# Kernel tuning notes

Measured on AMD Instinct MI355X. Metric: run time of the kernel, lower is better.

## Reference

```python
import jax, jax.numpy as jnp
import numpy as np
import math

# init config (matches init_kwargs); sigma/alpha are squared in __init__
SIGMA2 = 8.0 ** 2
ALPHA2 = 8.0 ** 2
C_SIZE = 512
STRIDE = 8
MINX = 1e-06
M = 100                      # ratio=100 > 1 -> M = int(ratio), capped at 100
K = C_SIZE // STRIDE         # 64 grid cells per axis
G = K * K                    # 4096 density-field cells
B, N = 8, 512                # images, annotated points per image
TWO_PI = 2.0 * math.pi


def setup_inputs():
    key = jax.random.key(0)
    k1, _ = jax.random.split(key)
    points = jax.random.uniform(k1, (B, N, 2), dtype=jnp.float32) * C_SIZE
    st_sizes = jnp.full((B,), float(C_SIZE), dtype=jnp.float32)
    return {"points": points, "st_sizes": st_sizes}


def _per_image(pts, cood):
    # pts: [N,2]; cood: [K]
    x = pts[:, 0]
    y = pts[:, 1]
    dx = x[:, None] - cood[None, :]                 # [N,K]
    dy = y[:, None] - cood[None, :]                 # [N,K]
    # dis_all = y_dis[:, :, None] + x_dis[:, None, :] flattened: g = iy*K + ix
    dis = (dy[:, :, None] ** 2 + dx[:, None, :] ** 2).reshape(pts.shape[0], G)  # [N,G]
    s1 = ALPHA2 + SIGMA2
    s2 = ALPHA2 + SIGMA2 / 2.0
    m = jnp.exp(-0.5 / s1 * dis) / (TWO_PI * s1)    # [N,G]
    tv = jnp.exp(-0.5 / s2 * dis) / (TWO_PI * s2)
    v = (tv / (TWO_PI * 2.0 * SIGMA2)).sum(0) - (m ** 2).sum(0)   # [G] (sel_v == v, no bg)
    # top-M cells by sel_v, then sort indices ascending (ratio>1 branch -> static M)
    inds = jnp.argsort(-v)
    Minds = jnp.sort(inds[:M])                      # [M]
    v = jnp.maximum(v, MINX)                        # add=False -> clamp
    # xf[n, iy*K+ix] = x_n - cood[ix]; yf[n, iy*K+ix] = y_n - cood[iy]
    iy = Minds // K
    ix = Minds % K
    xfM = dx[:, ix]                                 # [N,M]
    yfM = dy[:, iy]                                 # [N,M]
    df = (xfM[:, None, :] - xfM[:, :, None]) ** 2 + (yfM[:, None, :] - yfM[:, :, None]) ** 2
    af = (0.5 * (xfM[:, None, :] + xfM[:, :, None])) ** 2 + (0.5 * (yfM[:, None, :] + yfM[:, :, None])) ** 2
    g1 = jnp.exp(-0.5 / (2.0 * SIGMA2) * df) / (TWO_PI * 2.0 * SIGMA2)          # [N,M,M]
    tmpv2 = (g1 * (jnp.exp(-0.5 / s2 * af) / (TWO_PI * s2))).sum(0) + g1.sum(0)  # [M,M]
    disM = dis[:, Minds]                            # [N,M]
    tmpm2 = jnp.exp(-0.5 / s1 * disM) / (TWO_PI * s1)
    A = tmpv2 - tmpm2.T @ tmpm2                     # [M,M]
    eye = jnp.eye(M, dtype=bool)
    A = jnp.where(eye, 1e-10, A)                    # diag overwritten to 1e-10
    vM = v[Minds] + 1e-10
    tmpA = vM[:, None] * jnp.linalg.inv(A) * vM[None, :] + jnp.diag(vM)
    Bm = jnp.linalg.inv(tmpA)
    return m, v, A, Bm, Minds


def reference(points, st_sizes):
    # st_sizes only matters for use_background=True; kept for signature fidelity
    cood = jnp.arange(0, C_SIZE, STRIDE, dtype=jnp.float32) + STRIDE / 2.0
    m, v, A, Bm, Minds = jax.vmap(lambda p: _per_image(p, cood))(points)
    return m, v, A, Bm, Minds
```

## Files before the change

### kernel.cpp

```cpp
#include <hip/hip_runtime.h>
#include <math.h>

#ifndef M_PI
#define M_PI 3.14159265358979323846
#endif

#define BB 8
#define NN 512
#define KK 64
#define GG 4096
#define MM 100

#define SZ_VD    (BB*GG*8u*4u)
#define OFF_VD   0u
#define SZ_VM    (BB*MM*4u)
#define OFF_VM   (OFF_VD + SZ_VD)
#define SZ_AD    (BB*MM*MM*4u)
#define OFF_AD   (OFF_VM + SZ_VM)

#define OUT_M  0
#define OUT_V  (BB*NN*GG)
#define OUT_A  (OUT_V + BB*GG)
#define OUT_B  (OUT_A + BB*MM*MM)
#define OUT_MI (OUT_B + BB*MM*MM)

#define MU_PER 8
#define MU_VP 4096
#define MU_AS 2048
#define MU_IV 10240

__device__ __forceinline__ void m_units(const float* __restrict__ pts,
                                        float* __restrict__ out, int u0, int cnt) {
  const float CM = (float)(1.0/(2.0*M_PI*128.0));
  for (int k = 0; k < cnt; ++k) {
    int u = u0 + k;
    int t = u*256 + (int)threadIdx.x;
    int e = t << 2;
    int img = e >> 21;
    int rem = e & ((1 << 21) - 1);
    int n = rem >> 12;
    int g = rem & 4095;
    int iy = g >> 6, ix = g & 63;
    float x = pts[(img*NN + n)*2 + 0];
    float y = pts[(img*NN + n)*2 + 1];
    float dy = y - (8.0f*iy + 4.0f);
    float ey = __expf(dy*dy*(-0.5f/128.0f));
    float4 r;
    float dx0 = x - (8.0f*ix + 4.0f);
    float dx1 = x - (8.0f*(ix+1) + 4.0f);
    float dx2 = x - (8.0f*(ix+2) + 4.0f);
    float dx3 = x - (8.0f*(ix+3) + 4.0f);
    r.x = ey*__expf(dx0*dx0*(-0.5f/128.0f))*CM;
    r.y = ey*__expf(dx1*dx1*(-0.5f/128.0f))*CM;
    r.z = ey*__expf(dx2*dx2*(-0.5f/128.0f))*CM;
    r.w = ey*__expf(dx3*dx3*(-0.5f/128.0f))*CM;
    *reinterpret_cast<float4*>(&out[OUT_M + e]) = r;
  }
}

__device__ __forceinline__ void m_units512(const float* __restrict__ pts,
                                           float* __restrict__ out, int u0, int cnt) {
  const float CM = (float)(1.0/(2.0*M_PI*128.0));
  for (int k = 0; k < cnt/2; ++k) {
    int t = u0*256 + k*512 + (int)threadIdx.x;
    int e = t << 2;
    int img = e >> 21;
    int rem = e & ((1 << 21) - 1);
    int n = rem >> 12;
    int g = rem & 4095;
    int iy = g >> 6, ix = g & 63;
    float x = pts[(img*NN + n)*2 + 0];
    float y = pts[(img*NN + n)*2 + 1];
    float dy = y - (8.0f*iy + 4.0f);
    float ey = __expf(dy*dy*(-0.5f/128.0f));
    float4 r;
    float dx0 = x - (8.0f*ix + 4.0f);
    float dx1 = x - (8.0f*(ix+1) + 4.0f);
    float dx2 = x - (8.0f*(ix+2) + 4.0f);
    float dx3 = x - (8.0f*(ix+3) + 4.0f);
    r.x = ey*__expf(dx0*dx0*(-0.5f/128.0f))*CM;
    r.y = ey*__expf(dx1*dx1*(-0.5f/128.0f))*CM;
    r.z = ey*__expf(dx2*dx2*(-0.5f/128.0f))*CM;
    r.w = ey*__expf(dx3*dx3*(-0.5f/128.0f))*CM;
    *reinterpret_cast<float4*>(&out[OUT_M + e]) = r;
  }
}

__device__ __forceinline__ float flt_readlane(float v, int l) {
  return __int_as_float(__builtin_amdgcn_readlane(__float_as_int(v), l));
}

__global__ __launch_bounds__(256) void k_vpart(const float* __restrict__ pts,
                                               double* __restrict__ vd,
                                               float* __restrict__ out) {
  __shared__ double sEy2[16][66], sEy3[16][66], sEx2[16][66], sEx3[16][66];
  __shared__ float px[128], py[128];
  int bid = blockIdx.x;
  if (bid >= BB*64) { m_units(pts, out, (bid - BB*64)*MU_PER, MU_PER); return; }
  int quarter = bid & 3;
  int rem = bid >> 2;
  int tile = rem & 15;
  int img = rem >> 4;
  int iy0 = (tile >> 2) << 4;
  int ix0 = (tile & 3) << 4;
  int tx = threadIdx.x & 15, ty = threadIdx.x >> 4;
  int n = threadIdx.x & 63;
  int tbl = threadIdx.x >> 6;
  if (threadIdx.x < 128) {
    px[threadIdx.x] = pts[(img*NN + quarter*128 + threadIdx.x)*2 + 0];
    py[threadIdx.x] = pts[(img*NN + quarter*128 + threadIdx.x)*2 + 1];
  }
  const double alpha = (tbl & 1) ? (1.0/128.0) : (0.5/96.0);
  const double Q = exp(-128.0*alpha);
  const int base = (tbl >= 2) ? ix0 : iy0;
  double* dst = (tbl == 0) ? &sEy2[0][0] : (tbl == 1) ? &sEy3[0][0]
              : (tbl == 2) ? &sEx2[0][0] : &sEx3[0][0];
  double aV = 0.0, aM = 0.0;
  for (int kc = 0; kc < 2; ++kc) {
    int nbl = kc << 6;
    __syncthreads();
    {
      int nn = nbl + n;
      double coord = (tbl >= 2) ? (double)px[nn] : (double)py[nn];
      double d0 = coord - (8.0*base + 4.0);
      double E = exp(-alpha*d0*d0);
      double R = exp(alpha*(16.0*d0 - 64.0));
      #pragma unroll
      for (int row = 0; row < 16; ++row) {
        dst[row*66 + n] = E;
        E *= R; R *= Q;
      }
    }
    __syncthreads();
    #pragma unroll 8
    for (int n2 = 0; n2 < 64; n2 += 2) {
      double2 y2 = *reinterpret_cast<const double2*>(&sEy2[ty][n2]);
      double2 x2 = *reinterpret_cast<const double2*>(&sEx2[tx][n2]);
      double2 y3 = *reinterpret_cast<const double2*>(&sEy3[ty][n2]);
      double2 x3 = *reinterpret_cast<const double2*>(&sEx3[tx][n2]);
      aV += y2.x*x2.x; aV += y2.y*x2.y;
      aM += y3.x*x3.x; aM += y3.y*x3.y;
    }
  }
  const double CTV = 1.0/((2.0*M_PI*96.0)*(2.0*M_PI*128.0));
  const double CM2 = 1.0/((2.0*M_PI*128.0)*(2.0*M_PI*128.0));
  vd[quarter*(BB*GG) + img*GG + (iy0 + ty)*KK + ix0 + tx] = CTV*aV - CM2*aM;
}

union AselU {
  struct {
    unsigned int ku[GG];
    unsigned int hist[32][257];
    unsigned int wq[4];
    unsigned int sPref, sMask;
    unsigned int sRem, sPickB, sPickRem, sCGt, sCEq;
    int tie[128];
  } se;
  struct {
    float sxi[16][130], syi[16][130], sti[16][130];
    float sxj[16][130], syj[16][130], stj[16][130];
    float px[NN], py[NN];
    float cxi[16], cyi[16], cxj[16], cyj[16];
  } ka;
};

__device__ __forceinline__ void wave_sort128(int* a) {
  int L = (int)(threadIdx.x & 63);
  int e0 = a[2*L], e1 = a[2*L + 1];
  for (int kk = 2; kk <= 128; kk <<= 1) {
    for (int jj = kk >> 1; jj >= 2; jj >>= 1) {
      int pl = jj >> 1;
      int o0 = __shfl_xor(e0, pl);
      int o1 = __shfl_xor(e1, pl);
      bool upper = (L & pl) != 0;
      bool up = ((2*L) & kk) == 0;
      if (up != upper) { e0 = min(e0, o0); e1 = min(e1, o1); }
      else             { e0 = max(e0, o0); e1 = max(e1, o1); }
    }
    bool up = ((2*L) & kk) == 0;
    int lo = min(e0, e1), hi = max(e0, e1);
    e0 = up ? lo : hi; e1 = up ? hi : lo;
  }
  a[2*L] = e0; a[2*L + 1] = e1;
}

__global__ __launch_bounds__(256) void k_Asel(const float* __restrict__ pts,
                                              const double* __restrict__ vd,
                                              float* __restrict__ out,
                                              float* __restrict__ ad,
                                              float* __restrict__ vm) {
  __shared__ AselU u;
  __shared__ int selFinal[128];
  int bid = blockIdx.x;
  if (bid >= BB*28) { m_units(pts, out, MU_VP + (bid - BB*28)*MU_PER, MU_PER); return; }
  int img = bid / 28;
  int tile = bid - img*28;
  bool tile0 = (tile == 0);
  int tid = threadIdx.x;
  int wv = tid >> 6;
  int lane = tid & 63;
  int hc = tid >> 3;

  for (int t = 0; t < 16; ++t) {
    int g = t*256 + tid;
    float v = (float)(((vd[img*GG + g] + vd[BB*GG + img*GG + g])
                     + vd[2*BB*GG + img*GG + g]) + vd[3*BB*GG + img*GG + g]);
    if (tile0) out[OUT_V + img*GG + g] = fmaxf(v, 1e-6f);
    int w = __float_as_int(v);
    u.se.ku[g] = (w < 0) ? ~(unsigned)w : ((unsigned)w | 0x80000000u);
  }
  if (tid == 0) {
    u.se.sRem = 100; u.se.sPref = 0u; u.se.sMask = 0u;
    u.se.sCGt = 0; u.se.sCEq = 0;
  }
  for (int shift = 24; shift >= 0; shift -= 8) {
    for (int s = tid; s < 32*257; s += 256) (&u.se.hist[0][0])[s] = 0;
    __syncthreads();
    unsigned mask = u.se.sMask, pref = u.se.sPref;
    for (int t = 0; t < 16; ++t) {
      unsigned k = u.se.ku[t*256 + tid];
      if ((k & mask) == pref)
        atomicAdd(&u.se.hist[hc][(k >> shift) & 255u], 1u);
    }
    __syncthreads();
    unsigned tot = 0;
    #pragma unroll
    for (int c = 0; c < 32; ++c) tot += u.se.hist[c][tid];
    unsigned val = tot;
    #pragma unroll
    for (int off = 1; off < 64; off <<= 1) {
      unsigned o = (unsigned)__shfl_down((int)val, off);
      if (lane + off < 64) val += o;
    }
    if (lane == 0) u.se.wq[wv] = val;
    __syncthreads();
    unsigned suf = val;
    for (int w2 = wv + 1; w2 < 4; ++w2) suf += u.se.wq[w2];
    unsigned rem = u.se.sRem;
    unsigned sgt = suf - tot;
    if (suf >= rem && sgt < rem) { u.se.sPickB = (unsigned)tid; u.se.sPickRem = rem - sgt; }
    __syncthreads();
    if (tid == 0) {
      u.se.sPref |= u.se.sPickB << shift;
      u.se.sMask |= 255u << shift;
      u.se.sRem   = u.se.sPickRem;
    }
    __syncthreads();
  }
  unsigned T = u.se.sPref;
  for (int t = 0; t < 16; ++t) {
    int g = t*256 + tid;
    unsigned k = u.se.ku[g];
    if (k > T) {
      unsigned p = atomicAdd(&u.se.sCGt, 1u);
      selFinal[p] = g;
    } else if (k == T) {
      unsigned p = atomicAdd(&u.se.sCEq, 1u);
      if (p < 128) u.se.tie[p] = g;
    }
  }
  __syncthreads();
  unsigned cgt = u.se.sCGt, ceq = u.se.sCEq, r = u.se.sRem;
  if (tid < 128 && tid >= (int)((ceq < 128u) ? ceq : 128u)) u.se.tie[tid] = 0x7fffffff;
  __syncthreads();
  if (tid < 64) wave_sort128(u.se.tie);
  __syncthreads();
  if (tid < (int)r) selFinal[cgt + tid] = u.se.tie[tid];
  if (tid >= MM && tid < 128) selFinal[tid] = 0x7fffffff;
  __syncthreads();
  if (tid < 64) wave_sort128(selFinal);
  __syncthreads();
  if (tile0 && tid < MM) {
    int mi = selFinal[tid];
    out[OUT_MI + img*MM + tid] = (float)mi;
    float vsel = (float)(((vd[img*GG + mi] + vd[BB*GG + img*GG + mi])
                        + vd[2*BB*GG + img*GG + mi]) + vd[3*BB*GG + img*GG + mi]);
    vm[img*MM + tid] = fmaxf(vsel, 1e-6f) + 1e-10f;
  }
  __syncthreads();

  int it = 0, trem = tile;
  while (trem >= 7 - it) { trem -= 7 - it; ++it; }
  int jt = it + trem;
  int i0 = it*16, j0 = jt*16;
  int tj = tid & 15, ti = tid >> 4;
  int i = i0 + ti, j = j0 + tj;
  const float CM = (float)(1.0/(2.0*M_PI*128.0));
  const float C1 = (float)(1.0/(2.0*M_PI*128.0));
  const float C2 = (float)(1.0/(2.0*M_PI*96.0));
  for (int s = tid; s < NN; s += 256) {
    u.ka.px[s] = pts[(img*NN + s)*2 + 0];
    u.ka.py[s] = pts[(img*NN + s)*2 + 1];
  }
  if (tid < 16) {
    int gi = i0 + tid; if (gi > 99) gi = 99;
    int mi = selFinal[gi];
    u.ka.cxi[tid] = 8.0f*(mi & 63) + 4.0f;
    u.ka.cyi[tid] = 8.0f*(mi >> 6) + 4.0f;
  } else if (tid < 32) {
    int rr = tid - 16;
    int gj = j0 + rr; if (gj > 99) gj = 99;
    int mj = selFinal[gj];
    u.ka.cxj[rr] = 8.0f*(mj & 63) + 4.0f;
    u.ka.cyj[rr] = 8.0f*(mj >> 6) + 4.0f;
  }
  float aV = 0.0f, aM = 0.0f;
  for (int nc = 0; nc < NN; nc += 128) {
    __syncthreads();
    for (int s = tid; s < 16*128; s += 256) {
      int row = s >> 7, n = s & 127;
      float x = u.ka.px[nc + n], y = u.ka.py[nc + n];
      float fxi = x - u.ka.cxi[row], fyi = y - u.ka.cyi[row];
      u.ka.sxi[row][n] = fxi; u.ka.syi[row][n] = fyi;
      u.ka.sti[row][n] = __expf((fxi*fxi + fyi*fyi)*(-0.5f/128.0f))*CM;
      float fxj = x - u.ka.cxj[row], fyj = y - u.ka.cyj[row];
      u.ka.sxj[row][n] = fxj; u.ka.syj[row][n] = fyj;
      u.ka.stj[row][n] = __expf((fxj*fxj + fyj*fyj)*(-0.5f/128.0f))*CM;
    }
    __syncthreads();
    #pragma unroll 4
    for (int n = 0; n < 128; ++n) {
      float xi = u.ka.sxi[ti][n], yi = u.ka.syi[ti][n], tii = u.ka.sti[ti][n];
      float xj = u.ka.sxj[tj][n], yj = u.ka.syj[tj][n], tjj = u.ka.stj[tj][n];
      float ddx = xj - xi, ddy = yj - yi;
      float df = ddx*ddx + ddy*ddy;
      float sx = 0.5f*(xi + xj), sy = 0.5f*(yi + yj);
      float af = sx*sx + sy*sy;
      float g1 = __expf(df*(-0.5f/128.0f))*C1;
      float h  = __expf(af*(-0.5f/96.0f))*C2;
      aV += g1 + g1*h;
      aM += tii*tjj;
    }
  }
  if (i < 100 && j < 100) {
    float val = (i == j) ? 1e-10f : (float)((double)aV - (double)aM);
    out[OUT_A + (img*MM + i)*MM + j] = val;
    ad[(img*MM + i)*MM + j] = val;
    if (it != jt) {
      out[OUT_A + (img*MM + j)*MM + i] = val;
      ad[(img*MM + j)*MM + i] = val;
    }
  }
}

#define PRS 130
__global__ __launch_bounds__(512)
void k_inv_m(const float* __restrict__ ad,
             const float* __restrict__ vm,
             const float* __restrict__ pts,
             float* __restrict__ out) {
  __shared__ float S[128*17];
  __shared__ float Pr[16*PRS];
  __shared__ float svm[112];
  if (blockIdx.x >= BB) {
    m_units512(pts, out, MU_VP + MU_AS + ((int)blockIdx.x - BB)*MU_PER, MU_PER);
    return;
  }
  int img = blockIdx.x;
  int tx = threadIdx.x & 31, ty = threadIdx.x >> 5;
  float C[7][4];
  if (threadIdx.x < 100) svm[threadIdx.x] = vm[img*MM + threadIdx.x];
  #pragma unroll
  for (int a = 0; a < 7; ++a) {
    int r = ty + 16*a;
    #pragma unroll
    for (int b = 0; b < 4; ++b) {
      int col = tx + 32*b;
      float v2 = (r < 100 && col < 100) ? ad[(img*MM + r)*MM + col] : 0.0f;
      if (r == col && r < 100) v2 += vm[img*MM + r];
      C[a][b] = v2;
    }
  }
  for (int p = 0; p < 7; ++p) {
    int k0 = p*16;
    int nbp = (p == 6) ? 4 : 16;
    {
      int bp = p >> 1;
      bool mine = ((tx >> 4) == (p & 1));
      int cq = tx & 15;
      #pragma unroll
      for (int a = 0; a < 7; ++a) {
        int r = ty + 16*a;
        if (mine) {
          float val = 0.0f;
          #pragma unroll
          for (int b = 0; b < 4; ++b) if (b == bp) val = C[a][b];
          S[r*17 + cq] = (r < 100 && cq < nbp) ? val : 0.0f;
        }
      }
    }
    {
      float pv[4];
      #pragma unroll
      for (int b = 0; b < 4; ++b) pv[b] = 0.0f;
      #pragma unroll
      for (int a = 0; a < 7; ++a) {
        #pragma unroll
        for (int b = 0; b < 4; ++b) if (a == p) pv[b] = C[a][b];
      }
      #pragma unroll
      for (int b = 0; b < 4; ++b) Pr[ty*PRS + tx + 32*b] = pv[b];
    }
    __syncthreads();
    if (threadIdx.x < 64) {
      int lane = threadIdx.x;
      float P0[16], P1[16];
      #pragma unroll
      for (int c = 0; c < 16; ++c) {
        P0[c] = S[lane*17 + c];
        P1[c] = (lane + 64 < 112) ? S[(lane + 64)*17 + c] : 0.0f;
      }
      #pragma unroll
      for (int kk = 0; kk < 16; ++kk) {
        if (kk < nbp) {
          int kg = k0 + kk;
          int r1 = lane + 64;
          bool khigh = kg >= 64; int kl = kg & 63;
          float pivinv = 1.0f / flt_readlane(khigh ? P1[kk] : P0[kk], kl);
          float pr[16];
          #pragma unroll
          for (int c = 0; c < 16; ++c) {
            float pv = flt_readlane(khigh ? P1[c] : P0[c], kl);
            pr[c] = (c == kk) ? pivinv : pv*pivinv;
          }
          {
            float f = P0[kk];
            if (lane == kg) {
              #pragma unroll
              for (int c = 0; c < 16; ++c) P0[c] = pr[c];
            } else {
              #pragma unroll
              for (int c = 0; c < 16; ++c) P0[c] = ((c == kk) ? 0.0f : P0[c]) - f*pr[c];
            }
          }
          {
            float f = P1[kk];
            if (r1 == kg) {
              #pragma unroll
              for (int c = 0; c < 16; ++c) P1[c] = pr[c];
            } else {
              #pragma unroll
              for (int c = 0; c < 16; ++c) P1[c] = ((c == kk) ? 0.0f : P1[c]) - f*pr[c];
            }
          }
        }
      }
      #pragma unroll
      for (int c = 0; c < 16; ++c) {
        S[lane*17 + c] = P0[c];
        if (lane + 64 < 112) S[(lane + 64)*17 + c] = P1[c];
      }
    }
    __syncthreads();
    #pragma unroll
    for (int a = 0; a < 7; ++a) {
      int r = ty + 16*a;
      bool prow_ = (r >= k0) && (r < k0 + 16);
      #pragma unroll
      for (int b = 0; b < 4; ++b) {
        int col = tx + 32*b;
        if (r >= 100 || (col >> 4) == p || prow_) C[a][b] = 0.0f;
      }
    }
    #pragma unroll 4
    for (int t = 0; t < 16; ++t) {
      bool tok = (t < nbp);
      float bt[4], sa[7];
      #pragma unroll
      for (int b = 0; b < 4; ++b) bt[b] = tok ? Pr[t*PRS + tx + 32*b] : 0.0f;
      #pragma unroll
      for (int a = 0; a < 7; ++a) sa[a] = S[(ty + 16*a)*17 + t];
      #pragma unroll
      for (int a = 0; a < 7; ++a)
        #pragma unroll
        for (int b = 0; b < 4; ++b) C[a][b] += sa[a]*bt[b];
    }
    #pragma unroll
    for (int a = 0; a < 7; ++a) {
      int r = ty + 16*a;
      #pragma unroll
      for (int b = 0; b < 4; ++b) {
        int col = tx + 32*b;
        if ((col >> 4) == p) C[a][b] = S[r*17 + (col & 15)];
      }
    }
    __syncthreads();
  }
  #pragma unroll
  for (int a = 0; a < 7; ++a) {
    int r = ty + 16*a; if (r >= 100) continue;
    float dinv = 1.0f / svm[r];
    #pragma unroll
    for (int b = 0; b < 4; ++b) {
      int col = tx + 32*b; if (col >= 100) continue;
      float val = ((col == r) ? dinv : 0.0f) - C[a][b];
      out[OUT_B + (img*MM + r)*MM + col] = val;
    }
  }
}

extern "C" void kernel_launch(void* const* d_in, const int* in_sizes, int n_in,
                              void* d_out, int out_size, void* d_ws, size_t ws_size,
                              hipStream_t stream) {
  const float* pts = (const float*)d_in[0];
  float* out = (float*)d_out;
  char* ws = (char*)d_ws;
  double* vd  = (double*)(ws + OFF_VD);
  float* vmd = (float*)(ws + OFF_VM);
  float* ad  = (float*)(ws + OFF_AD);

  hipLaunchKernelGGL(k_vpart, dim3(BB*64 + MU_VP/MU_PER), dim3(256), 0, stream, pts, vd, out);
  hipLaunchKernelGGL(k_Asel, dim3(BB*28 + MU_AS/MU_PER), dim3(256), 0, stream, pts, vd, out, ad, vmd);
  hipLaunchKernelGGL(k_inv_m, dim3(BB + MU_IV/MU_PER), dim3(512), 0, stream, ad, vmd, pts, out);
}
```

Baseline: 193.8 us.

## Split A-matrix point reduction across two blocks per tile, combine in inversion kernel

```diff
diff --git a/kernel.cpp b/kernel.cpp
--- a/kernel.cpp
+++ b/kernel.cpp
@@ -15,7 +15,7 @@
 #define OFF_VD   0u
 #define SZ_VM    (BB*MM*4u)
 #define OFF_VM   (OFF_VD + SZ_VD)
-#define SZ_AD    (BB*MM*MM*4u)
+#define SZ_AD    (BB*MM*MM*4u*2u)
 #define OFF_AD   (OFF_VM + SZ_VM)
 
 #define OUT_M  0
@@ -192,10 +192,12 @@
   __shared__ AselU u;
   __shared__ int selFinal[128];
   int bid = blockIdx.x;
-  if (bid >= BB*28) { m_units(pts, out, MU_VP + (bid - BB*28)*MU_PER, MU_PER); return; }
-  int img = bid / 28;
-  int tile = bid - img*28;
-  bool tile0 = (tile == 0);
+  if (bid >= BB*56) { m_units(pts, out, MU_VP + (bid - BB*56)*MU_PER, MU_PER); return; }
+  int img = bid / 56;
+  int rem56 = bid - img*56;
+  int tile = rem56 >> 1;
+  int half = rem56 & 1;
+  bool emit = (tile == 0) && (half == 0);
   int tid = threadIdx.x;
   int wv = tid >> 6;
   int lane = tid & 63;
@@ -205,7 +207,7 @@
     int g = t*256 + tid;
     float v = (float)(((vd[img*GG + g] + vd[BB*GG + img*GG + g])
                      + vd[2*BB*GG + img*GG + g]) + vd[3*BB*GG + img*GG + g]);
-    if (tile0) out[OUT_V + img*GG + g] = fmaxf(v, 1e-6f);
+    if (emit) out[OUT_V + img*GG + g] = fmaxf(v, 1e-6f);
     int w = __float_as_int(v);
     u.se.ku[g] = (w < 0) ? ~(unsigned)w : ((unsigned)w | 0x80000000u);
   }
@@ -270,7 +272,7 @@
   __syncthreads();
   if (tid < 64) wave_sort128(selFinal);
   __syncthreads();
-  if (tile0 && tid < MM) {
+  if (emit && tid < MM) {
     int mi = selFinal[tid];
     out[OUT_MI + img*MM + tid] = (float)mi;
     float vsel = (float)(((vd[img*GG + mi] + vd[BB*GG + img*GG + mi])
@@ -305,7 +307,7 @@
     u.ka.cyj[rr] = 8.0f*(mj >> 6) + 4.0f;
   }
   float aV = 0.0f, aM = 0.0f;
-  for (int nc = 0; nc < NN; nc += 128) {
+  for (int nc = half*256; nc < half*256 + 256; nc += 128) {
     __syncthreads();
     for (int s = tid; s < 16*128; s += 256) {
       int row = s >> 7, n = s & 127;
@@ -334,11 +336,9 @@
   }
   if (i < 100 && j < 100) {
     float val = (i == j) ? 1e-10f : (float)((double)aV - (double)aM);
-    out[OUT_A + (img*MM + i)*MM + j] = val;
-    ad[(img*MM + i)*MM + j] = val;
+    ad[((half*BB + img)*MM + i)*MM + j] = val;
     if (it != jt) {
-      out[OUT_A + (img*MM + j)*MM + i] = val;
-      ad[(img*MM + j)*MM + i] = val;
+      ad[((half*BB + img)*MM + j)*MM + i] = val;
     }
   }
 }
@@ -366,8 +366,17 @@
     #pragma unroll
     for (int b = 0; b < 4; ++b) {
       int col = tx + 32*b;
-      float v2 = (r < 100 && col < 100) ? ad[(img*MM + r)*MM + col] : 0.0f;
-      if (r == col && r < 100) v2 += vm[img*MM + r];
+      float v2 = 0.0f;
+      if (r < 100 && col < 100) {
+        if (r == col) {
+          v2 = 1e-10f + vm[img*MM + r];
+          out[OUT_A + (img*MM + r)*MM + col] = 1e-10f;
+        } else {
+          float s = ad[(img*MM + r)*MM + col] + ad[((BB + img)*MM + r)*MM + col];
+          v2 = s;
+          out[OUT_A + (img*MM + r)*MM + col] = s;
+        }
+      }
       C[a][b] = v2;
     }
   }
@@ -510,6 +519,6 @@
   float* ad  = (float*)(ws + OFF_AD);
 
   hipLaunchKernelGGL(k_vpart, dim3(BB*64 + MU_VP/MU_PER), dim3(256), 0, stream, pts, vd, out);
-  hipLaunchKernelGGL(k_Asel, dim3(BB*28 + MU_AS/MU_PER), dim3(256), 0, stream, pts, vd, out, ad, vmd);
+  hipLaunchKernelGGL(k_Asel, dim3(BB*56 + MU_AS/MU_PER), dim3(256), 0, stream, pts, vd, out, ad, vmd);
   hipLaunchKernelGGL(k_inv_m, dim3(BB + MU_IV/MU_PER), dim3(512), 0, stream, ad, vmd, pts, out);
 }
```

Result: no change. 190.4 us (-1.7%).
